# Optimization experiments

Measured on AMD Instinct MI355X. Metric: run time of the kernel, lower is better.

The kernel has to match this reference:

```python
import jax, jax.numpy as jnp
import numpy as np

B, N, H, F = 4, 256, 192, 64
SUP = 1.0  # ancestor_suppression_strength
EPS = 1e-6


def setup_inputs() -> dict:
    key = jax.random.key(0)
    ks = jax.random.split(key, 14)
    z = jax.random.normal(ks[0], (B, H), jnp.float32)
    # strictly-lower-triangular 0/1 parent (link) matrix: row t lists parents j < t
    tri = jnp.tril(jnp.ones((N, N), jnp.float32), -1)
    targets = (jax.random.uniform(ks[1], (B, N, N)) < 0.05).astype(jnp.float32) * tri

    def w(k, shape):
        fan_in = shape[0]
        return jax.random.normal(k, shape, jnp.float32) / jnp.sqrt(jnp.float32(fan_in))

    return {
        "z": z,
        "teacher_forcing_targets": targets,
        "W_init": w(ks[2], (H, H)), "b_init": jnp.zeros((H,), jnp.float32),
        "W_ih": w(ks[3], (H, 3 * H)), "W_hh": w(ks[4], (H, 3 * H)),
        "b_ih": jnp.zeros((3 * H,), jnp.float32), "b_hh": jnp.zeros((3 * H,), jnp.float32),
        "W1": w(ks[5], (3 * H, H)), "b1": jnp.zeros((H,), jnp.float32),
        "W2": w(ks[6], (H, 1)), "b2": jnp.zeros((1,), jnp.float32),
        "Wf": w(ks[7], (H, F)), "bf": jnp.zeros((F,), jnp.float32),
        "atom_count": N,
    }


def gru_cell(x, h, W_ih, W_hh, b_ih, b_hh):
    gx = x @ W_ih + b_ih
    gh = h @ W_hh + b_hh
    xr, xu, xn = jnp.split(gx, 3, axis=-1)
    hr, hu, hn = jnp.split(gh, 3, axis=-1)
    r = jax.nn.sigmoid(xr + hr)
    u = jax.nn.sigmoid(xu + hu)
    n = jnp.tanh(xn + r * hn)
    return (1.0 - u) * n + u * h


def reference(z, teacher_forcing_targets, W_init, b_init, W_ih, W_hh, b_ih, b_hh,
              W1, b1, W2, b2, Wf, bf, atom_count):
    b, n = teacher_forcing_targets.shape[0], teacher_forcing_targets.shape[1]
    h = z.shape[-1]
    idx = jnp.arange(n)

    # decoder_init: latent z -> hidden state of node 0
    h0 = jnp.tanh(z @ W_init + b_init)
    S0 = jnp.zeros((b, n, h), z.dtype).at[:, 0].set(h0)   # node states
    A0 = jnp.zeros((b, n, n), z.dtype)                    # ancestor indicator A[b,i,j]=1 iff j ancestor of i

    def step(carry, xs):
        S, A, ll = carry
        t, tgt = xs                                   # t scalar, tgt (B,N) = parents of node t
        mask = (idx < t).astype(S.dtype)              # existing nodes
        cnt = jnp.maximum(mask.sum(), 1.0)
        # mean-aggregation over existing node states -> GRU message
        m = (S * mask[None, :, None]).sum(axis=1) / cnt              # (B,H)
        h_prov = gru_cell(m, z, W_ih, W_hh, b_ih, b_hh)              # provisional state of new node
        # parent logits: MLP([h_new, h_existing, z]) per candidate parent
        feats = jnp.concatenate([
            jnp.broadcast_to(h_prov[:, None, :], S.shape), S,
            jnp.broadcast_to(z[:, None, :], S.shape)], axis=-1)      # (B,N,3H)
        logits = (jax.nn.relu(feats @ W1 + b1) @ W2 + b2)[..., 0]    # (B,N)
        # ancestor suppression: suppress j if j is already an ancestor of one of t's parents
        reach = jnp.einsum('bn,bnm->bm', tgt, A)
        anc = (reach > 0).astype(S.dtype)
        p = jax.nn.sigmoid(logits) * (1.0 - SUP * anc)
        p = jnp.clip(p, EPS, 1.0 - EPS)
        ll = ll + (mask[None, :] * (tgt * jnp.log(p) + (1.0 - tgt) * jnp.log1p(-p))).sum()
        # teacher forcing: commit parents, update new-node state from parent states
        deg = jnp.maximum(tgt.sum(axis=-1, keepdims=True), 1.0)
        msg = jnp.einsum('bn,bnh->bh', tgt, S) / deg
        h_new = gru_cell(msg, h_prov, W_ih, W_hh, b_ih, b_hh)
        S = jax.lax.dynamic_update_slice(S, h_new[:, None, :], (0, t, 0))
        row = jnp.minimum(tgt + anc, 1.0)             # ancestors(t) = parents U ancestors(parents)
        A = jax.lax.dynamic_update_slice(A, row[:, None, :], (0, t, 0))
        return (S, A, ll), None

    ts = jnp.arange(1, n)
    tgt_rows = jnp.swapaxes(teacher_forcing_targets[:, 1:, :], 0, 1)  # (N-1,B,N)
    (S, A, ll), _ = jax.lax.scan(step, (S0, A0, jnp.zeros((), z.dtype)), (ts, tgt_rows))

    L = teacher_forcing_targets            # teacher-forced link matrix
    node_features = S @ Wf + bf            # node_feature_decoder head
    return L, node_features, ll
```

## Files before the change

kernel.cpp:

```cpp
#include <hip/hip_runtime.h>
#include <stdint.h>

#define B_ 4
#define N_ 256
#define H_ 192
#define H3_ 576
#define F_ 64

#define H0_OFF   0u
#define ZC_OFF   1024u
#define HL_OFF   2048u
#define SL_OFF   395264u
#define AN_OFF   788480u
#define TG_OFF   796672u
#define PL_OFF   804864u
#define PC_OFF   870400u
#define DG_OFF   871424u
#define D_OFF    872448u
#define G_OFF    1462272u
#define C_OFF    1658880u
#define FHL_OFF  1855488u
#define FSL_OFF  2248704u
#define XC_OFF   2641920u

#define AN64 (AN_OFF/2)
#define TG64 (TG_OFF/2)

#define NF_OUT 262144u
#define LL_OUT 327680u

__device__ __forceinline__ float sigm_(float x){ return 1.0f/(1.0f + __expf(-x)); }
__device__ __forceinline__ float tanh_(float x){
  float ax = fabsf(x);
  float e = __expf(-2.0f*ax);
  float t = (1.0f - e)/(1.0f + e);
  return x < 0.0f ? -t : t;
}

__device__ __forceinline__ void st_mall_(uint32_t* p, unsigned long long u){
  __hip_atomic_store((unsigned long long*)p, u, __ATOMIC_RELAXED, __HIP_MEMORY_SCOPE_AGENT);
}
__device__ __forceinline__ unsigned long long ld_mall_(const uint32_t* p){
  return __hip_atomic_load((const unsigned long long*)p, __ATOMIC_RELAXED, __HIP_MEMORY_SCOPE_AGENT);
}
__device__ __forceinline__ unsigned long long ld_l2_(const uint32_t* p){
  unsigned long long v;
  asm volatile("buffer_inv sc0\n\t"
               "s_waitcnt vmcnt(0)\n\t"
               "global_load_dwordx2 %0, %1, off\n\t"
               "s_waitcnt vmcnt(0)"
               : "=v"(v) : "v"(p) : "memory");
  return v;
}
__device__ __forceinline__ void pubF_(uint32_t* fp, float v, uint32_t tag){
  unsigned long long u = ((unsigned long long)tag<<32) | (unsigned long long)__float_as_uint(v);
  __hip_atomic_store((unsigned long long*)fp, u, __ATOMIC_RELAXED, __HIP_MEMORY_SCOPE_WORKGROUP);
}
__device__ __forceinline__ void pub2_(uint32_t* fp, uint32_t* mp, float v, uint32_t tag){
  unsigned long long u = ((unsigned long long)tag<<32) | (unsigned long long)__float_as_uint(v);
  __hip_atomic_store((unsigned long long*)fp, u, __ATOMIC_RELAXED, __HIP_MEMORY_SCOPE_WORKGROUP);
  st_mall_(mp, u);
}
__device__ __forceinline__ void mirror_(const uint32_t* fp, uint32_t* mp, uint32_t tag){
  unsigned long long x;
  do {
    x = __hip_atomic_load((const unsigned long long*)fp, __ATOMIC_RELAXED, __HIP_MEMORY_SCOPE_WORKGROUP);
  } while ((uint32_t)(x>>32) != tag);
  st_mall_(mp, x);
}
__device__ __forceinline__ float pollH_(const uint32_t* fp, const uint32_t* mp, int fast, uint32_t tag){
  unsigned long long x = 0; int it = 0;
  for(;;){
    if (fast){
      x = ld_l2_(fp);
      if ((uint32_t)(x>>32) != tag && (((++it) & 3) == 3)){
        unsigned long long m = ld_mall_(mp);
        if ((uint32_t)(m>>32) == tag) x = m;
      }
    } else {
      x = ld_mall_(mp);
    }
    if (__all((int)((uint32_t)(x>>32) == tag))) break;
  }
  return __uint_as_float((uint32_t)x);
}
__device__ __forceinline__ void bar_(){
  asm volatile("s_waitcnt lgkmcnt(0)" ::: "memory");
  __builtin_amdgcn_s_barrier();
  asm volatile("" ::: "memory");
}

__global__ void __launch_bounds__(192) k_pre1(const float* __restrict__ z,
    const float* __restrict__ Winit, const float* __restrict__ binit,
    const float* __restrict__ W1, const float* __restrict__ b1,
    const float* __restrict__ tgt, float* ws, float* out)
{
  int bx = blockIdx.x, b = blockIdx.y, tid = threadIdx.x;
  if (bx == N_){
    __shared__ float zs[H_];
    zs[tid] = z[b*H_ + tid];
    __syncthreads();
    float a0=0.f, a1=0.f;
    for (int k=0;k<H_;k++){
      float zv = zs[k];
      a0 += zv * Winit[(size_t)k*H_ + tid];
      a1 += zv * W1[(size_t)(2*H_ + k)*H_ + tid];
    }
    ws[H0_OFF + b*H_ + tid] = tanh_(a0 + binit[tid]);
    ws[ZC_OFF + b*H_ + tid] = a1 + b1[tid];
    if (b==0 && tid==0) out[LL_OUT] = 0.0f;
    return;
  }
  if (tid >= 64) return;
  int t = bx, lane = tid;
  uint32_t* wsu = (uint32_t*)ws;
  unsigned long long* ws64 = (unsigned long long*)ws;
  const float* row = tgt + ((size_t)(b*N_) + t)*N_;
  uint8_t* pl = ((uint8_t*)&wsu[PL_OFF]) + (size_t)(b*N_ + t)*N_;
  int cnt = 0;
  #pragma unroll
  for (int m=0;m<4;m++){
    float v = row[m*64 + lane];
    bool p = (v != 0.0f);
    unsigned long long bw = __ballot(p);
    if (lane == 0) ws64[TG64 + (size_t)(b*N_+t)*4 + m] = bw;
    if (p){
      int pos = cnt + (int)__popcll(bw & ((1ULL<<lane)-1ULL));
      pl[pos] = (uint8_t)(m*64 + lane);
    }
    cnt += (int)__popcll(bw);
  }
  if (lane == 0){
    wsu[PC_OFF + b*N_ + t] = (uint32_t)cnt;
    ws[DG_OFF + b*N_ + t] = 1.0f / fmaxf((float)cnt, 1.0f);
  }
}

__global__ void __launch_bounds__(512, 1) k_pass1(const float* __restrict__ z,
    const float* __restrict__ Wih, const float* __restrict__ Whh,
    const float* __restrict__ bih_g, const float* __restrict__ bhh_g,
    float* ws)
{
  int bx = blockIdx.x;
  int b = bx & 7;
  if (b >= B_) return;
  int blk = bx >> 3;
  int tid = threadIdx.x;
  const int e  = tid >> 3;
  const int kc = tid & 7;
  const int E  = blk*64 + e;

  float* wsf = ws;
  uint32_t* wsu = (uint32_t*)ws;
  unsigned long long* ws64 = (unsigned long long*)ws;

  __shared__ __align__(16) float sh[H_];
  __shared__ __align__(16) float ss[H_];
  __shared__ float sDG[N_], sTF1[N_];
  __shared__ uint32_t sPC[N_];
  __shared__ int sfast[4];
  __shared__ unsigned long long sAB[N_][4];

  {
    float v = wsf[H0_OFF + b*H_ + E];
    if (kc == 0)
      pub2_(&wsu[FSL_OFF + (unsigned)(b*N_)*384u + 2u*(unsigned)E],
            &wsu[SL_OFF  + (unsigned)(b*N_)*384u + 2u*(unsigned)E], v, 1u);
    if (kc == 1) ss[E] = v;
  }

  uint32_t xcc = (uint32_t)__builtin_amdgcn_s_getreg((31u<<11) | 20u) & 15u;
  if (tid == 0)
    __hip_atomic_store(&wsu[XC_OFF + b*16 + blk], 0xC0DE0000u | xcc,
                       __ATOMIC_RELAXED, __HIP_MEMORY_SCOPE_AGENT);
  if (tid < 64){
    uint32_t v = 0; int ok;
    do {
      v = (tid < 3) ? __hip_atomic_load(&wsu[XC_OFF + b*16 + tid],
              __ATOMIC_RELAXED, __HIP_MEMORY_SCOPE_AGENT) : (0xC0DE0000u | xcc);
      ok = (int)((v >> 16) == 0xC0DEu);
    } while (!__all(ok));
    if (tid < 3) sfast[tid] = ((v & 0xFFu) == xcc) ? 1 : 0;
  }

  for (int i = tid; i < N_; i += 512){
    sDG[i] = wsf[DG_OFF + b*N_ + i];
    sPC[i] = wsu[PC_OFF + b*N_ + i];
    float f1 = 0.f;
    if (i >= 1){
      unsigned long long w1 = ws64[TG64 + (size_t)(b*N_+i)*4 + ((i-1)>>6)];
      f1 = (float)((w1 >> ((i-1)&63)) & 1ULL);
    }
    sTF1[i] = f1;
  }
  if (blk == 0 && tid >= 192 && tid < 196) sAB[0][tid-192] = 0ULL;

  float rwih[3][24], rwhh[3][24], rbih[3], rbhh[3], rghz[3];
  #pragma unroll
  for (int g=0; g<3; g++){
    int col = g*H_ + E;
    #pragma unroll
    for (int i=0;i<24;i++){
      rwih[g][i] = Wih[(size_t)(kc*24+i)*H3_ + col];
      rwhh[g][i] = Whh[(size_t)(kc*24+i)*H3_ + col];
    }
    rbih[g] = bih_g[col];
    rbhh[g] = bhh_g[col];
  }
  {
    float a0=0.f,a1=0.f,a2=0.f;
    #pragma unroll
    for (int i=0;i<24;i++){
      float zv = z[b*H_ + kc*24 + i];
      a0 += zv*rwhh[0][i]; a1 += zv*rwhh[1][i]; a2 += zv*rwhh[2][i];
    }
    #pragma unroll
    for (int m=1;m<8;m<<=1){
      a0 += __shfl_xor(a0,m); a1 += __shfl_xor(a1,m); a2 += __shfl_xor(a2,m);
    }
    rghz[0]=a0+rbhh[0]; rghz[1]=a1+rbhh[1]; rghz[2]=a2+rbhh[2];
  }
  float zreg = z[b*H_ + E];

  __syncthreads();
  if (tid < 128){
    int j = (tid < blk*64) ? tid : tid + 64;
    ss[j] = pollH_(&wsu[FSL_OFF + (unsigned)(b*N_)*384u + 2u*(unsigned)j],
                   &wsu[SL_OFF  + (unsigned)(b*N_)*384u + 2u*(unsigned)j],
                   sfast[j>>6], 1u);
  }
  __syncthreads();

  float q0=0.f, q1=0.f, q2=0.f;
  const uint8_t* plbase = ((const uint8_t*)&wsu[PL_OFF]) + (size_t)(b*N_)*N_;
  float* Dbase = wsf + D_OFF + (size_t)((b*3+blk)*N_)*H_;

  for (int t=1; t<N_; t++){
    const uint32_t tagH = (uint32_t)(t+1);
    float d0=0.f,d1=0.f,d2=0.f;
    #pragma unroll
    for (int c=0;c<6;c++){
      float4 v4 = *(const float4*)&ss[kc*24 + c*4];
      float xx0=v4.x, xx1=v4.y, xx2=v4.z, xx3=v4.w;
      d0 += xx0*rwih[0][c*4+0]; d1 += xx0*rwih[1][c*4+0]; d2 += xx0*rwih[2][c*4+0];
      d0 += xx1*rwih[0][c*4+1]; d1 += xx1*rwih[1][c*4+1]; d2 += xx1*rwih[2][c*4+1];
      d0 += xx2*rwih[0][c*4+2]; d1 += xx2*rwih[1][c*4+2]; d2 += xx2*rwih[2][c*4+2];
      d0 += xx3*rwih[0][c*4+3]; d1 += xx3*rwih[1][c*4+3]; d2 += xx3*rwih[2][c*4+3];
    }
    #pragma unroll
    for (int m=1;m<8;m<<=1){
      d0 += __shfl_xor(d0,m); d1 += __shfl_xor(d1,m); d2 += __shfl_xor(d2,m);
    }
    q0 += d0; q1 += d1; q2 += d2;
    float invt = 1.0f/(float)t;
    float r = sigm_(q0*invt + rbih[0] + rghz[0]);
    float u = sigm_(q1*invt + rbih[1] + rghz[1]);
    float n = tanh_(q2*invt + rbih[2] + r*rghz[2]);
    float hp = (1.0f-u)*n + u*zreg;
    if (kc == 0){
      pubF_(&wsu[FHL_OFF + (unsigned)(b*N_+t)*384u + 2u*(unsigned)E], hp, tagH);
      float* Dr = Dbase + (size_t)(t-1)*H_;
      Dr[e] = d0; Dr[64+e] = d1; Dr[128+e] = d2;
    }
    if (kc == 1) sh[E] = hp;
    float ga0=0.f, ga1=0.f, ga2=0.f;
    {
      int pc = (int)sPC[t];
      const uint8_t* pl = plbase + (size_t)t*N_;
      for (int i=kc; i<pc; i+=8){
        int p = pl[i];
        if (p == t-1) continue;
        const float* Dp = Dbase + (size_t)p*H_;
        ga0 += Dp[e]; ga1 += Dp[64+e]; ga2 += Dp[128+e];
      }
    }
    #pragma unroll
    for (int m=1;m<8;m<<=1){
      ga0 += __shfl_xor(ga0,m); ga1 += __shfl_xor(ga1,m); ga2 += __shfl_xor(ga2,m);
    }
    if (tid < 128){
      int j = (tid < blk*64) ? tid : tid + 64;
      sh[j] = pollH_(&wsu[FHL_OFF + (unsigned)(b*N_+t)*384u + 2u*(unsigned)j],
                     &wsu[HL_OFF  + (unsigned)(b*N_+t)*384u + 2u*(unsigned)j],
                     sfast[j>>6], tagH);
    } else if (tid < 192){
      int ml = tid - 128;
      unsigned em = (unsigned)(blk*64 + ml);
      mirror_(&wsu[FHL_OFF + (unsigned)(b*N_+t)*384u + 2u*em],
              &wsu[HL_OFF  + (unsigned)(b*N_+t)*384u + 2u*em], tagH);
    } else if (blk == 0 && tid < 208){
      int lane16 = tid - 192;
      int ip = lane16 >> 2, w = lane16 & 3;
      int pc = (int)sPC[t];
      const uint8_t* pl = plbase + (size_t)t*N_;
      unsigned long long acc = 0ULL;
      for (int i=ip; i<pc; i+=4) acc |= sAB[pl[i]][w];
      acc |= __shfl_xor(acc, 4);
      acc |= __shfl_xor(acc, 8);
      if (ip == 0){
        ws64[AN64 + (size_t)(b*N_+t)*4 + w] = acc;
        sAB[t][w] = acc | ws64[TG64 + (size_t)(b*N_+t)*4 + w];
      }
    }
    bar_();
    float y0=0.f,y1=0.f,y2=0.f;
    #pragma unroll
    for (int c=0;c<6;c++){
      float4 v4 = *(const float4*)&sh[kc*24 + c*4];
      float xx0=v4.x, xx1=v4.y, xx2=v4.z, xx3=v4.w;
      y0 += xx0*rwhh[0][c*4+0]; y1 += xx0*rwhh[1][c*4+0]; y2 += xx0*rwhh[2][c*4+0];
      y0 += xx1*rwhh[0][c*4+1]; y1 += xx1*rwhh[1][c*4+1]; y2 += xx1*rwhh[2][c*4+1];
      y0 += xx2*rwhh[0][c*4+2]; y1 += xx2*rwhh[1][c*4+2]; y2 += xx2*rwhh[2][c*4+2];
      y0 += xx3*rwhh[0][c*4+3]; y1 += xx3*rwhh[1][c*4+3]; y2 += xx3*rwhh[2][c*4+3];
    }
    #pragma unroll
    for (int m=1;m<8;m<<=1){
      y0 += __shfl_xor(y0,m); y1 += __shfl_xor(y1,m); y2 += __shfl_xor(y2,m);
    }
    float dginv = sDG[t], tf1 = sTF1[t];
    float gxa = (ga0 + tf1*d0)*dginv + rbih[0];
    float gxb = (ga1 + tf1*d1)*dginv + rbih[1];
    float gxc = (ga2 + tf1*d2)*dginv + rbih[2];
    float r2 = sigm_(gxa + y0 + rbhh[0]);
    float u2 = sigm_(gxb + y1 + rbhh[1]);
    float n2 = tanh_(gxc + r2*(y2 + rbhh[2]));
    float hn = (1.0f-u2)*n2 + u2*hp;
    if (kc == 0)
      pubF_(&wsu[FSL_OFF + (unsigned)(b*N_+t)*384u + 2u*(unsigned)E], hn, tagH);
    if (kc == 1) ss[E] = hn;
    if (tid < 128){
      int j = (tid < blk*64) ? tid : tid + 64;
      ss[j] = pollH_(&wsu[FSL_OFF + (unsigned)(b*N_+t)*384u + 2u*(unsigned)j],
                     &wsu[SL_OFF  + (unsigned)(b*N_+t)*384u + 2u*(unsigned)j],
                     sfast[j>>6], tagH);
    } else if (tid >= 192 && tid < 256){
      int ml = tid - 192;
      unsigned em = (unsigned)(blk*64 + ml);
      mirror_(&wsu[FSL_OFF + (unsigned)(b*N_+t)*384u + 2u*em],
              &wsu[SL_OFF  + (unsigned)(b*N_+t)*384u + 2u*em], tagH);
    }
    bar_();
  }
}

__global__ void k_p2a(const float* __restrict__ W1, const float* __restrict__ Wf,
    const float* __restrict__ bf, float* ws, float* out)
{
  int j = blockIdx.x, b = blockIdx.y, tid = threadIdx.x;
  __shared__ float srow[H_], hrow[H_];
  __shared__ float nfp[3][F_];
  srow[tid] = ws[SL_OFF + (unsigned)(b*N_+j)*384u + 2u*tid];
  hrow[tid] = ws[HL_OFF + (unsigned)(b*N_+j)*384u + 2u*tid];
  __syncthreads();
  float accG = 0.f, accC = 0.f;
  for (int k=0;k<H_;k++){
    float sv = srow[k], hv = hrow[k];
    accG += sv * W1[(size_t)(H_+k)*H_ + tid];
    accC += hv * W1[(size_t)k*H_ + tid];
  }
  ws[G_OFF + ((size_t)b*H_ + tid)*N_ + j] = accG;
  ws[C_OFF + (size_t)(b*N_+j)*H_ + tid] = accC + ws[ZC_OFF + b*H_ + tid];
  int f = tid & 63, kp = tid >> 6;
  float a = 0.f;
  for (int i=0;i<64;i++){ int k = kp*64 + i; a += srow[k]*Wf[(size_t)k*F_ + f]; }
  nfp[kp][f] = a;
  __syncthreads();
  if (tid < F_) out[NF_OUT + (size_t)(b*N_+j)*F_ + tid] = nfp[0][tid]+nfp[1][tid]+nfp[2][tid] + bf[tid];
}

__global__ void __launch_bounds__(256) k_p2b(const float* __restrict__ W2,
    const float* __restrict__ b2p, float* ws, float* out)
{
  int t = blockIdx.x + 1, b = blockIdx.y;
  int tid = threadIdx.x; int lane = tid & 63; int wv = tid >> 6;
  __shared__ float cv[H_], w2s[H_];
  __shared__ float wsum[4];
  unsigned long long* ws64 = (unsigned long long*)ws;
  if (tid < H_){
    cv[tid] = ws[C_OFF + (size_t)(b*N_+t)*H_ + tid];
    w2s[tid] = W2[tid];
  }
  __syncthreads();
  float acc = 0.f;
  if (tid < t){
    const float* GT = ws + G_OFF + (size_t)b*H_*N_;
    float a = 0.f;
    for (int k=0;k<H_;k++) a += fmaxf(cv[k] + GT[(size_t)k*N_ + tid], 0.f) * w2s[k];
    float logit = a + b2p[0];
    float pp = 1.0f/(1.0f+__expf(-logit));
    unsigned long long an = ws64[AN64 + (size_t)(b*N_+t)*4 + (tid>>6)];
    unsigned long long tg = ws64[TG64 + (size_t)(b*N_+t)*4 + (tid>>6)];
    float anc = (float)((an >> (tid&63)) & 1ULL);
    pp = pp * (1.0f - anc);
    pp = fminf(fmaxf(pp, 1e-6f), 1.0f - 1e-6f);
    int tgb = (int)((tg >> (tid&63)) & 1ULL);
    acc = tgb ? logf(pp) : log1pf(-pp);
  }
  #pragma unroll
  for (int m=32;m>=1;m>>=1) acc += __shfl_xor(acc, m);
  if (lane == 0) wsum[wv] = acc;
  __syncthreads();
  if (tid == 0) atomicAdd(out + LL_OUT, wsum[0]+wsum[1]+wsum[2]+wsum[3]);
}

extern "C" void kernel_launch(void* const* d_in, const int* in_sizes, int n_in,
                              void* d_out, int out_size, void* d_ws, size_t ws_size,
                              hipStream_t stream) {
  (void)in_sizes; (void)n_in; (void)out_size; (void)ws_size;
  const float* z     = (const float*)d_in[0];
  const float* tgt   = (const float*)d_in[1];
  const float* Winit = (const float*)d_in[2];
  const float* binit = (const float*)d_in[3];
  const float* Wih   = (const float*)d_in[4];
  const float* Whh   = (const float*)d_in[5];
  const float* bih   = (const float*)d_in[6];
  const float* bhh   = (const float*)d_in[7];
  const float* W1    = (const float*)d_in[8];
  const float* b1    = (const float*)d_in[9];
  const float* W2    = (const float*)d_in[10];
  const float* b2    = (const float*)d_in[11];
  const float* Wf    = (const float*)d_in[12];
  const float* bf    = (const float*)d_in[13];
  float* out = (float*)d_out;
  float* ws  = (float*)d_ws;

  hipMemcpyAsync(d_out, d_in[1], (size_t)B_*N_*N_*sizeof(float), hipMemcpyDeviceToDevice, stream);

  k_pre1<<<dim3(N_+1, B_), dim3(192), 0, stream>>>(z, Winit, binit, W1, b1, tgt, ws, out);
  k_pass1<<<dim3(24), dim3(512), 0, stream>>>(z, Wih, Whh, bih, bhh, ws);
  k_p2a<<<dim3(N_, B_), dim3(H_), 0, stream>>>(W1, Wf, bf, ws, out);
  k_p2b<<<dim3(N_-1, B_), dim3(256), 0, stream>>>(W2, b2, ws, out);
}
```

Measured before the change: 1.069 ms.

## Replace polling mirror threads with direct wave-coalesced publish and non-temporal polls

Each block now writes its new hidden slice to shared memory, takes a block barrier, and then one wavefront publishes the tagged values coalesced to the fast buffer while another writes them directly to the agent-scope mirror buffer. This replaces mirror threads that spun on the fast copy before re-storing it. The fast-path poll load also drops the explicit cache invalidate and uses a non-temporal load instead. The aim is lower latency on the per-step cross-block exchange, at the cost of two extra block barriers per step and a dependence on the nt load actually seeing fresh data without the invalidate.

```diff
diff --git a/kernel.cpp b/kernel.cpp
--- a/kernel.cpp
+++ b/kernel.cpp
@@ -45,9 +45,7 @@
 }
 __device__ __forceinline__ unsigned long long ld_l2_(const uint32_t* p){
   unsigned long long v;
-  asm volatile("buffer_inv sc0\n\t"
-               "s_waitcnt vmcnt(0)\n\t"
-               "global_load_dwordx2 %0, %1, off\n\t"
+  asm volatile("global_load_dwordx2 %0, %1, off nt\n\t"
                "s_waitcnt vmcnt(0)"
                : "=v"(v) : "v"(p) : "memory");
   return v;
@@ -60,13 +58,6 @@
   unsigned long long u = ((unsigned long long)tag<<32) | (unsigned long long)__float_as_uint(v);
   __hip_atomic_store((unsigned long long*)fp, u, __ATOMIC_RELAXED, __HIP_MEMORY_SCOPE_WORKGROUP);
   st_mall_(mp, u);
-}
-__device__ __forceinline__ void mirror_(const uint32_t* fp, uint32_t* mp, uint32_t tag){
-  unsigned long long x;
-  do {
-    x = __hip_atomic_load((const unsigned long long*)fp, __ATOMIC_RELAXED, __HIP_MEMORY_SCOPE_WORKGROUP);
-  } while ((uint32_t)(x>>32) != tag);
-  st_mall_(mp, x);
 }
 __device__ __forceinline__ float pollH_(const uint32_t* fp, const uint32_t* mp, int fast, uint32_t tag){
   unsigned long long x = 0; int it = 0;
@@ -149,6 +140,8 @@
   const int e  = tid >> 3;
   const int kc = tid & 7;
   const int E  = blk*64 + e;
+  const int wv = tid >> 6;
+  const int l6 = tid & 63;
 
   float* wsf = ws;
   uint32_t* wsu = (uint32_t*)ws;
@@ -258,11 +251,15 @@
     float n = tanh_(q2*invt + rbih[2] + r*rghz[2]);
     float hp = (1.0f-u)*n + u*zreg;
     if (kc == 0){
-      pubF_(&wsu[FHL_OFF + (unsigned)(b*N_+t)*384u + 2u*(unsigned)E], hp, tagH);
       float* Dr = Dbase + (size_t)(t-1)*H_;
       Dr[e] = d0; Dr[64+e] = d1; Dr[128+e] = d2;
     }
     if (kc == 1) sh[E] = hp;
+    bar_();
+    if (wv == 2){
+      unsigned em = (unsigned)(blk*64 + l6);
+      pubF_(&wsu[FHL_OFF + (unsigned)(b*N_+t)*384u + 2u*em], sh[em], tagH);
+    }
     float ga0=0.f, ga1=0.f, ga2=0.f;
     {
       int pc = (int)sPC[t];
@@ -278,19 +275,19 @@
     for (int m=1;m<8;m<<=1){
       ga0 += __shfl_xor(ga0,m); ga1 += __shfl_xor(ga1,m); ga2 += __shfl_xor(ga2,m);
     }
+    if (wv == 3){
+      unsigned em = (unsigned)(blk*64 + l6);
+      unsigned long long u64v = ((unsigned long long)tagH<<32) |
+                                (unsigned long long)__float_as_uint(sh[em]);
+      st_mall_(&wsu[HL_OFF + (unsigned)(b*N_+t)*384u + 2u*em], u64v);
+    }
     if (tid < 128){
       int j = (tid < blk*64) ? tid : tid + 64;
       sh[j] = pollH_(&wsu[FHL_OFF + (unsigned)(b*N_+t)*384u + 2u*(unsigned)j],
                      &wsu[HL_OFF  + (unsigned)(b*N_+t)*384u + 2u*(unsigned)j],
                      sfast[j>>6], tagH);
-    } else if (tid < 192){
-      int ml = tid - 128;
-      unsigned em = (unsigned)(blk*64 + ml);
-      mirror_(&wsu[FHL_OFF + (unsigned)(b*N_+t)*384u + 2u*em],
-              &wsu[HL_OFF  + (unsigned)(b*N_+t)*384u + 2u*em], tagH);
-    } else if (blk == 0 && tid < 208){
-      int lane16 = tid - 192;
-      int ip = lane16 >> 2, w = lane16 & 3;
+    } else if (blk == 0 && wv == 4 && l6 < 16){
+      int ip = l6 >> 2, w = l6 & 3;
       int pc = (int)sPC[t];
       const uint8_t* pl = plbase + (size_t)t*N_;
       unsigned long long acc = 0ULL;
@@ -325,19 +322,22 @@
     float u2 = sigm_(gxb + y1 + rbhh[1]);
     float n2 = tanh_(gxc + r2*(y2 + rbhh[2]));
     float hn = (1.0f-u2)*n2 + u2*hp;
-    if (kc == 0)
-      pubF_(&wsu[FSL_OFF + (unsigned)(b*N_+t)*384u + 2u*(unsigned)E], hn, tagH);
     if (kc == 1) ss[E] = hn;
+    bar_();
+    if (wv == 2){
+      unsigned em = (unsigned)(blk*64 + l6);
+      pubF_(&wsu[FSL_OFF + (unsigned)(b*N_+t)*384u + 2u*em], ss[em], tagH);
+    } else if (wv == 3){
+      unsigned em = (unsigned)(blk*64 + l6);
+      unsigned long long u64v = ((unsigned long long)tagH<<32) |
+                                (unsigned long long)__float_as_uint(ss[em]);
+      st_mall_(&wsu[SL_OFF + (unsigned)(b*N_+t)*384u + 2u*em], u64v);
+    }
     if (tid < 128){
       int j = (tid < blk*64) ? tid : tid + 64;
       ss[j] = pollH_(&wsu[FSL_OFF + (unsigned)(b*N_+t)*384u + 2u*(unsigned)j],
                      &wsu[SL_OFF  + (unsigned)(b*N_+t)*384u + 2u*(unsigned)j],
                      sfast[j>>6], tagH);
-    } else if (tid >= 192 && tid < 256){
-      int ml = tid - 192;
-      unsigned em = (unsigned)(blk*64 + ml);
-      mirror_(&wsu[FSL_OFF + (unsigned)(b*N_+t)*384u + 2u*em],
-              &wsu[SL_OFF  + (unsigned)(b*N_+t)*384u + 2u*em], tagH);
     }
     bar_();
   }
```

Result: faster. 1.013 ms (-5.2%).
